# Optimization experiments

Measured on AMD Instinct MI355X. Metric: run time of the kernel, lower is better.

Reference implementation:

```python
import jax, jax.numpy as jnp
import numpy as np

B, N, K, G = 8, 16384, 16, 4
D_OUT = 128
CQ = CV = 64            # cv must equal d_out//2 for the lpe reshape to work
CQG, CVG = CQ // G, CV // G
C_LPE = D_OUT // (2 * G)  # = CVG = 16
BN_EPS = 1e-5


def setup_inputs() -> dict:
    key = jax.random.key(0)
    ks = jax.random.split(key, 8)
    xyz = jax.random.normal(ks[0], (B, N, 3), dtype=jnp.float32)
    query = jax.random.normal(ks[1], (B, CQ, N), dtype=jnp.float32)
    value = jax.random.normal(ks[2], (B, CV, N, 1), dtype=jnp.float32)
    neigh_idx = jax.random.randint(ks[3], (B, N, K), 0, N, dtype=jnp.int64)
    idx_base = (jnp.arange(B, dtype=jnp.int64) * N).reshape(B, 1, 1)
    lpe_W = jax.random.normal(ks[4], (C_LPE, 10), dtype=jnp.float32) * 0.1
    lpe_b = jnp.zeros((C_LPE,), dtype=jnp.float32)
    bn_gamma = jnp.ones((C_LPE,), dtype=jnp.float32)
    bn_beta = jnp.zeros((C_LPE,), dtype=jnp.float32)
    bn_mean = jnp.zeros((C_LPE,), dtype=jnp.float32)
    bn_var = jnp.ones((C_LPE,), dtype=jnp.float32)
    return {"xyz": xyz, "query": query, "value": value,
            "neigh_idx": neigh_idx, "idx_base": idx_base,
            "lpe_W": lpe_W, "lpe_b": lpe_b, "bn_gamma": bn_gamma,
            "bn_beta": bn_beta, "bn_mean": bn_mean, "bn_var": bn_var}


def _gtl_forward(xyz, query, value, neigh_idx, idx_base,
                 lpe_W, lpe_b, bn_gamma, bn_beta, bn_mean, bn_var):
    b, n, _ = xyz.shape
    k = neigh_idx.shape[-1]
    lq = query.reshape(b, G, CQG, n)                       # [b,g,cqg,n]
    lv = value.reshape(b, G, CVG, n)                       # [b,g,cvg,n]
    xyz_g = jnp.broadcast_to(xyz[:, None].transpose(0, 1, 3, 2), (b, G, 3, n))
    # temp channels: key(cqg) | value(cvg) | xyz(3)
    temp = jnp.concatenate([lq, lv, xyz_g], axis=2)        # [b,g,c,n]
    c = temp.shape[2]
    # flat gather honoring idx_base (batch offsets into b*n)
    flat_idx = (neigh_idx + idx_base).reshape(-1)          # [b*n*k]
    pc_flat = temp.transpose(1, 0, 3, 2).reshape(G, b * n, c)
    feat = pc_flat[:, flat_idx, :].reshape(G, b, n, k, c)
    feat = feat.transpose(1, 0, 4, 2, 3)                   # [b,g,c,n,k]
    lk = feat[:, :, :CQG]                                  # [b,g,cqg,n,k]
    lv_n = feat[:, :, CQG:CQG + CVG]                       # [b,g,cvg,n,k]
    f_xyz = feat[:, :, -3:]                                # [b,g,3,n,k]
    # relative positional encoding -> [b,g,n,k,10]
    neighbor_xyz = f_xyz.transpose(0, 1, 3, 4, 2)          # [b,g,n,k,3]
    xyz_tile = jnp.broadcast_to(xyz[:, None, :, None, :], (b, G, n, k, 3))
    relative_xyz = xyz_tile - neighbor_xyz
    relative_dis = jnp.sqrt(jnp.sum(relative_xyz ** 2, axis=-1, keepdims=True))
    relf = jnp.concatenate([relative_dis, relative_xyz, xyz_tile, neighbor_xyz], axis=-1)
    # permute(0,4,2,1,3) then merge (g,k) -> conv input [b,10,n,g*k]
    relf = relf.transpose(0, 4, 2, 1, 3).reshape(b, 10, n, G * k)
    y = jnp.einsum('oc,bcnm->bonm', lpe_W, relf) + lpe_b[None, :, None, None]
    inv_std = bn_gamma / jnp.sqrt(bn_var + BN_EPS)
    y = (y - bn_mean[None, :, None, None]) * inv_std[None, :, None, None] \
        + bn_beta[None, :, None, None]
    y = jax.nn.relu(y)
    f_enc = y.reshape(b, C_LPE, n, G, k).transpose(0, 3, 1, 2, 4)  # [b,g,cvg,n,k]
    # elementwise attention over neighbors
    la = jax.nn.softmax(jnp.sum(lq[..., None] * lk, axis=2), axis=-1)  # [b,g,n,k]
    lv_cat = jnp.concatenate([lv_n, f_enc], axis=2)        # [b,g,2*cvg,n,k]
    out = jnp.sum(la[:, :, None] * lv_cat, axis=-1).reshape(b, -1, n, 1)
    # attention centrality: scatter-add over neighbor indices
    idx_flat = jnp.broadcast_to(neigh_idx[:, None], (b, G, n, k)).reshape(b, G, n * k)
    att_flat = la.reshape(b, G, n * k)
    centrality = jnp.zeros((b, G, n), dtype=la.dtype).at[
        jnp.arange(b)[:, None, None], jnp.arange(G)[None, :, None], idx_flat
    ].add(att_flat)
    return out, f_enc, centrality


def reference(xyz, query, value, neigh_idx, idx_base,
              lpe_W, lpe_b, bn_gamma, bn_beta, bn_mean, bn_var):
    return _gtl_forward(xyz, query, value, neigh_idx, idx_base,
                        lpe_W, lpe_b, bn_gamma, bn_beta, bn_mean, bn_var)
```

## Files before the change

### kernel.cpp

```cpp
#include <hip/hip_runtime.h>
#include <hip/hip_fp16.h>

#define B_    8
#define N_    16384
#define K_    16
#define G_    4
#define CQ_   64
#define CV_   64
#define CQG_  16
#define CVG_  16
#define CLPE_ 16
#define NT_   (B_*G_*N_)

typedef float f4v __attribute__((ext_vector_type(4)));

static __device__ __forceinline__ void nt_store4(float* p, float a, float b,
                                                 float c, float d) {
    f4v v = {a, b, c, d};
    __builtin_nontemporal_store(v, (f4v*)p);
}
static __device__ __forceinline__ void nt_store1(float* p, float a) {
    __builtin_nontemporal_store(a, p);
}

union QV { uint4 u; __half2 h[4]; };

__global__ __launch_bounds__(256) void gtl_prep(
    const float* __restrict__ query,
    const float* __restrict__ value,
    const float* __restrict__ xyz,
    uint4*  __restrict__ qvT,
    float4* __restrict__ xyz4,
    float*  __restrict__ cent)
{
    const int gid = blockIdx.x * 256 + threadIdx.x;
    const int n   = gid & (N_ - 1);
    const int bg  = gid >> 14;
    const int g   = bg & (G_ - 1);
    const int b   = bg >> 2;

    const float* qb = query + (size_t)b*CQ_*N_ + (size_t)g*CQG_*N_ + n;
    const float* vb = value + (size_t)b*CV_*N_ + (size_t)g*CVG_*N_ + n;

    uint u[16];
    #pragma unroll
    for (int i = 0; i < 8; ++i) {
        const float a0 = qb[(size_t)(2*i+0)*N_];
        const float a1 = qb[(size_t)(2*i+1)*N_];
        const __half2 h = __floats2half2_rn(a0, a1);
        u[i] = *(const uint*)&h;
    }
    #pragma unroll
    for (int i = 0; i < 8; ++i) {
        const float a0 = vb[(size_t)(2*i+0)*N_];
        const float a1 = vb[(size_t)(2*i+1)*N_];
        const __half2 h = __floats2half2_rn(a0, a1);
        u[8+i] = *(const uint*)&h;
    }

    uint4* o = qvT + (size_t)gid * 4;
    o[0] = make_uint4(u[0],  u[1],  u[2],  u[3]);
    o[1] = make_uint4(u[4],  u[5],  u[6],  u[7]);
    o[2] = make_uint4(u[8],  u[9],  u[10], u[11]);
    o[3] = make_uint4(u[12], u[13], u[14], u[15]);

    cent[gid] = 0.f;

    if (g == 0) {
        const size_t pp = (size_t)b*N_ + n;
        xyz4[pp] = make_float4(xyz[pp*3+0], xyz[pp*3+1], xyz[pp*3+2], 0.f);
    }
}

__global__ __launch_bounds__(256) void gtl_main(
    const uint4*  __restrict__ qvT,
    const float4* __restrict__ xyz4,
    const int*    __restrict__ nidx,
    const float*  __restrict__ lpeW,
    const float*  __restrict__ lpeB,
    const float*  __restrict__ bnG,
    const float*  __restrict__ bnB,
    const float*  __restrict__ bnM,
    const float*  __restrict__ bnV,
    float* __restrict__ out,
    float* __restrict__ fenc,
    float* __restrict__ cent)
{
    __shared__ float4 sA[CLPE_];
    __shared__ float4 sB[CLPE_];

    const int t = threadIdx.x;
    if (t < CLPE_) {
        const float scale = bnG[t] * rsqrtf(bnV[t] + 1e-5f);
        const float shift = (lpeB[t] - bnM[t]) * scale + bnB[t];
        const float w0 = lpeW[t*10+0];
        const float w1 = lpeW[t*10+1], w2 = lpeW[t*10+2], w3 = lpeW[t*10+3];
        const float w4 = lpeW[t*10+4], w5 = lpeW[t*10+5], w6 = lpeW[t*10+6];
        const float w7 = lpeW[t*10+7], w8 = lpeW[t*10+8], w9 = lpeW[t*10+9];
        sA[t] = make_float4(scale*(w1+w4), scale*(w2+w5), scale*(w3+w6), shift);
        sB[t] = make_float4(scale*(w7-w1), scale*(w8-w2), scale*(w9-w3), scale*w0);
    }
    __syncthreads();

    const int wid  = blockIdx.x;
    const int xcd  = wid & 7;
    const int slot = wid >> 3;
    const int bg   = (xcd << 2) | (slot >> 6);
    const int n    = ((slot & 63) << 8) | t;
    const int b    = bg >> 2;

    int idx[K_];
    {
        const int4* ip = (const int4*)(nidx + (size_t)(b*N_ + n) * K_);
        #pragma unroll
        for (int q4 = 0; q4 < K_/4; ++q4) {
            const int4 v = ip[q4];
            idx[q4*4+0] = v.x; idx[q4*4+1] = v.y;
            idx[q4*4+2] = v.z; idx[q4*4+3] = v.w;
        }
    }

    const uint4* qvslab = qvT + (size_t)bg * N_ * 4;

    float lq[CQG_];
    {
        QV cA, cB;
        cA.u = qvslab[(size_t)n*4+0];
        cB.u = qvslab[(size_t)n*4+1];
        #pragma unroll
        for (int i = 0; i < 4; ++i) {
            const float2 f = __half22float2(cA.h[i]);
            lq[2*i+0] = f.x; lq[2*i+1] = f.y;
        }
        #pragma unroll
        for (int i = 0; i < 4; ++i) {
            const float2 f = __half22float2(cB.h[i]);
            lq[8+2*i+0] = f.x; lq[8+2*i+1] = f.y;
        }
    }

    float la[K_];
    #pragma unroll 4
    for (int k = 0; k < K_; ++k) {
        const uint4* qj = qvslab + (size_t)idx[k]*4;
        QV a, b2;
        a.u  = qj[0];
        b2.u = qj[1];
        float s = 0.f;
        #pragma unroll
        for (int i = 0; i < 4; ++i) {
            const float2 f = __half22float2(a.h[i]);
            s = fmaf(lq[2*i+0], f.x, s);
            s = fmaf(lq[2*i+1], f.y, s);
        }
        #pragma unroll
        for (int i = 0; i < 4; ++i) {
            const float2 f = __half22float2(b2.h[i]);
            s = fmaf(lq[8+2*i+0], f.x, s);
            s = fmaf(lq[8+2*i+1], f.y, s);
        }
        la[k] = s;
    }

    float m = la[0];
    #pragma unroll
    for (int k = 1; k < K_; ++k) m = fmaxf(m, la[k]);
    float ssum = 0.f;
    #pragma unroll
    for (int k = 0; k < K_; ++k) { const float e = __expf(la[k] - m); la[k] = e; ssum += e; }
    const float inv = 1.f / ssum;
    #pragma unroll
    for (int k = 0; k < K_; ++k) la[k] *= inv;

    {
        float* cb = cent + (size_t)bg * N_;
        #pragma unroll
        for (int k = 0; k < K_; ++k) atomicAdd(cb + idx[k], la[k]);
    }

    const float4 cpt = xyz4[(size_t)b*N_ + n];
    float basec[CLPE_];
    #pragma unroll
    for (int c = 0; c < CLPE_; ++c) {
        const float4 a = sA[c];
        basec[c] = fmaf(a.x, cpt.x, fmaf(a.y, cpt.y, fmaf(a.z, cpt.z, a.w)));
    }

    float4 nbr[K_];
    float accV[CVG_];
    #pragma unroll
    for (int c = 0; c < CVG_; ++c) accV[c] = 0.f;

    #pragma unroll 4
    for (int k = 0; k < K_; ++k) {
        const int j = idx[k];
        const float4 p = xyz4[(size_t)b*N_ + j];
        const float rx = cpt.x - p.x, ry = cpt.y - p.y, rz = cpt.z - p.z;
        const float d  = sqrtf(fmaf(rx,rx, fmaf(ry,ry, rz*rz)));
        nbr[k] = make_float4(p.x, p.y, p.z, d);
        const float w = la[k];
        const uint4* vj = qvslab + (size_t)j*4 + 2;
        QV v0, v1;
        v0.u = vj[0];
        v1.u = vj[1];
        #pragma unroll
        for (int i = 0; i < 4; ++i) {
            const float2 f = __half22float2(v0.h[i]);
            accV[2*i+0] = fmaf(w, f.x, accV[2*i+0]);
            accV[2*i+1] = fmaf(w, f.y, accV[2*i+1]);
        }
        #pragma unroll
        for (int i = 0; i < 4; ++i) {
            const float2 f = __half22float2(v1.h[i]);
            accV[8+2*i+0] = fmaf(w, f.x, accV[8+2*i+0]);
            accV[8+2*i+1] = fmaf(w, f.y, accV[8+2*i+1]);
        }
    }

    float* fe = fenc + ((size_t)bg * CLPE_ * N_ + n) * K_;
    float* ob = out  + (size_t)bg * (CVG_ + CLPE_) * N_ + n;

    #pragma unroll 2
    for (int c = 0; c < CLPE_; ++c) {
        const float4 wB = sB[c];
        const float base = basec[c];
        float e[K_];
        float acc = 0.f;
        #pragma unroll
        for (int k = 0; k < K_; ++k) {
            const float4 p = nbr[k];
            float tt = base;
            tt = fmaf(wB.x, p.x, tt);
            tt = fmaf(wB.y, p.y, tt);
            tt = fmaf(wB.z, p.z, tt);
            tt = fmaf(wB.w, p.w, tt);
            tt = fmaxf(tt, 0.f);
            e[k] = tt;
            acc  = fmaf(la[k], tt, acc);
        }
        float* fo = fe + (size_t)c * (N_ * K_);
        nt_store4(fo + 0,  e[0],  e[1],  e[2],  e[3]);
        nt_store4(fo + 4,  e[4],  e[5],  e[6],  e[7]);
        nt_store4(fo + 8,  e[8],  e[9],  e[10], e[11]);
        nt_store4(fo + 12, e[12], e[13], e[14], e[15]);
        nt_store1(ob + (size_t)(CVG_ + c) * N_, acc);
    }

    #pragma unroll
    for (int c = 0; c < CVG_; ++c) nt_store1(ob + (size_t)c * N_, accV[c]);
}

__global__ __launch_bounds__(256) void gtl_fallback(
    const float* __restrict__ xyz,
    const float* __restrict__ query,
    const float* __restrict__ value,
    const int*   __restrict__ nidx,
    const float* __restrict__ lpeW,
    const float* __restrict__ lpeB,
    const float* __restrict__ bnG,
    const float* __restrict__ bnB,
    const float* __restrict__ bnM,
    const float* __restrict__ bnV,
    float* __restrict__ out,
    float* __restrict__ fenc,
    float* __restrict__ cent)
{
    __shared__ float4 sA[CLPE_];
    __shared__ float4 sB[CLPE_];
    const int t = threadIdx.x;
    if (t < CLPE_) {
        const float scale = bnG[t] * rsqrtf(bnV[t] + 1e-5f);
        const float shift = (lpeB[t] - bnM[t]) * scale + bnB[t];
        const float w0 = lpeW[t*10+0];
        const float w1 = lpeW[t*10+1], w2 = lpeW[t*10+2], w3 = lpeW[t*10+3];
        const float w4 = lpeW[t*10+4], w5 = lpeW[t*10+5], w6 = lpeW[t*10+6];
        const float w7 = lpeW[t*10+7], w8 = lpeW[t*10+8], w9 = lpeW[t*10+9];
        sA[t] = make_float4(scale*(w1+w4), scale*(w2+w5), scale*(w3+w6), shift);
        sB[t] = make_float4(scale*(w7-w1), scale*(w8-w2), scale*(w9-w3), scale*w0);
    }
    __syncthreads();
    const int gid = blockIdx.x * 256 + t;
    const int n   = gid & (N_ - 1);
    const int bg  = gid >> 14;
    const int g   = bg & (G_ - 1);
    const int b   = bg >> 2;
    const float cx = xyz[(size_t)(b*N_ + n)*3 + 0];
    const float cy = xyz[(size_t)(b*N_ + n)*3 + 1];
    const float cz = xyz[(size_t)(b*N_ + n)*3 + 2];
    int idx[K_];
    const int4* ip = (const int4*)(nidx + (size_t)(b*N_ + n) * K_);
    #pragma unroll
    for (int q4 = 0; q4 < K_/4; ++q4) {
        const int4 v = ip[q4];
        idx[q4*4+0] = v.x; idx[q4*4+1] = v.y; idx[q4*4+2] = v.z; idx[q4*4+3] = v.w;
    }
    const float* qb = query + (size_t)b*CQ_*N_ + (size_t)g*CQG_*N_;
    float lq[CQG_];
    #pragma unroll
    for (int c = 0; c < CQG_; ++c) lq[c] = qb[(size_t)c*N_ + n];
    float la[K_];
    #pragma unroll 4
    for (int k = 0; k < K_; ++k) {
        const float* qj = qb + idx[k];
        float s = 0.f;
        #pragma unroll
        for (int c = 0; c < CQG_; ++c) s = fmaf(lq[c], qj[(size_t)c*N_], s);
        la[k] = s;
    }
    float m = la[0];
    #pragma unroll
    for (int k = 1; k < K_; ++k) m = fmaxf(m, la[k]);
    float ssum = 0.f;
    #pragma unroll
    for (int k = 0; k < K_; ++k) { const float e = __expf(la[k] - m); la[k] = e; ssum += e; }
    const float inv = 1.f / ssum;
    #pragma unroll
    for (int k = 0; k < K_; ++k) la[k] *= inv;
    float* cb = cent + (size_t)bg * N_;
    #pragma unroll
    for (int k = 0; k < K_; ++k) atomicAdd(cb + idx[k], la[k]);
    float basec[CLPE_];
    #pragma unroll
    for (int c = 0; c < CLPE_; ++c) {
        const float4 a = sA[c];
        basec[c] = fmaf(a.x, cx, fmaf(a.y, cy, fmaf(a.z, cz, a.w)));
    }
    const float* vb = value + (size_t)b*CV_*N_ + (size_t)g*CVG_*N_;
    float accV[CVG_], accE[CLPE_];
    #pragma unroll
    for (int c = 0; c < CLPE_; ++c) { accV[c] = 0.f; accE[c] = 0.f; }
    float* fe = fenc + ((size_t)bg * CLPE_ * N_ + n) * K_;
    #pragma unroll 2
    for (int k = 0; k < K_; ++k) {
        const int j = idx[k];
        const float nx = xyz[(size_t)(b*N_ + j)*3 + 0];
        const float ny = xyz[(size_t)(b*N_ + j)*3 + 1];
        const float nz = xyz[(size_t)(b*N_ + j)*3 + 2];
        const float rx = cx - nx, ry = cy - ny, rz = cz - nz;
        const float d  = sqrtf(rx*rx + ry*ry + rz*rz);
        const float w  = la[k];
        const float* vj = vb + j;
        #pragma unroll
        for (int c = 0; c < CLPE_; ++c) {
            const float4 bb = sB[c];
            float e = basec[c];
            e = fmaf(bb.x, nx, e); e = fmaf(bb.y, ny, e);
            e = fmaf(bb.z, nz, e); e = fmaf(bb.w, d,  e);
            e = fmaxf(e, 0.f);
            fe[(size_t)c*(N_*K_) + k] = e;
            accE[c] = fmaf(w, e, accE[c]);
            accV[c] = fmaf(w, vj[(size_t)c*N_], accV[c]);
        }
    }
    float* ob = out + (size_t)bg * (CVG_ + CLPE_) * N_ + n;
    #pragma unroll
    for (int c = 0; c < CVG_; ++c)  ob[(size_t)c*N_]        = accV[c];
    #pragma unroll
    for (int c = 0; c < CLPE_; ++c) ob[(size_t)(CVG_+c)*N_] = accE[c];
}

extern "C" void kernel_launch(void* const* d_in, const int* in_sizes, int n_in,
                              void* d_out, int out_size, void* d_ws, size_t ws_size,
                              hipStream_t stream) {
    (void)in_sizes; (void)n_in; (void)out_size;

    const float* xyz   = (const float*)d_in[0];
    const float* query = (const float*)d_in[1];
    const float* value = (const float*)d_in[2];
    const int*   nidx  = (const int*)  d_in[3];
    const float* lpeW  = (const float*)d_in[5];
    const float* lpeB  = (const float*)d_in[6];
    const float* bnG   = (const float*)d_in[7];
    const float* bnB   = (const float*)d_in[8];
    const float* bnM   = (const float*)d_in[9];
    const float* bnV   = (const float*)d_in[10];

    float* out  = (float*)d_out;
    float* fenc = out  + (size_t)B_ * (G_*(CVG_+CLPE_)) * N_;
    float* cent = fenc + (size_t)B_ * G_ * CLPE_ * N_ * K_;

    const size_t qv_bytes   = (size_t)NT_ * 64;
    const size_t xyz4_bytes = (size_t)B_ * N_ * sizeof(float4);
    const size_t need = qv_bytes + xyz4_bytes;

    const int grid = NT_ / 256;

    if (ws_size >= need) {
        uint4*  qvT  = (uint4*)d_ws;
        float4* xyz4 = (float4*)((char*)d_ws + qv_bytes);
        hipLaunchKernelGGL(gtl_prep, dim3(grid), dim3(256), 0, stream,
                           query, value, xyz, qvT, xyz4, cent);
        hipLaunchKernelGGL(gtl_main, dim3(grid), dim3(256), 0, stream,
                           qvT, xyz4, nidx, lpeW, lpeB, bnG, bnB, bnM, bnV,
                           out, fenc, cent);
    } else {
        hipMemsetAsync(cent, 0, sizeof(float) * (size_t)B_ * G_ * N_, stream);
        hipLaunchKernelGGL(gtl_fallback, dim3(grid), dim3(256), 0, stream,
                           xyz, query, value, nidx, lpeW, lpeB, bnG, bnB, bnM, bnV,
                           out, fenc, cent);
    }
}
```

Before: 1.204 ms.

## Fuse score and value gathers with online softmax, two points per thread

The main kernel now processes two point slots per thread with half the grid. It gathers each neighbor's full 64-byte q/v row plus xyz in one pass and uses an online-softmax rescale, so the value accumulation no longer needs a second gather loop. Neighbor coordinates and distances are kept as half2 to cut register use, neighbor indices are read with nontemporal loads, and the prep kernel's block-to-data mapping now matches the main kernel's XCD-aware layout. This trades extra exp and multiply work and some fp16 precision loss in the positional encoding for fewer memory passes and lower register pressure.

```diff
diff --git a/kernel.cpp b/kernel.cpp
--- a/kernel.cpp
+++ b/kernel.cpp
@@ -13,6 +13,7 @@
 #define NT_   (B_*G_*N_)
 
 typedef float f4v __attribute__((ext_vector_type(4)));
+typedef int   i4v __attribute__((ext_vector_type(4)));
 
 static __device__ __forceinline__ void nt_store4(float* p, float a, float b,
                                                  float c, float d) {
@@ -33,29 +34,32 @@
     float4* __restrict__ xyz4,
     float*  __restrict__ cent)
 {
-    const int gid = blockIdx.x * 256 + threadIdx.x;
-    const int n   = gid & (N_ - 1);
-    const int bg  = gid >> 14;
+    const int wid = blockIdx.x;
+    const int xcd = wid & 7;
+    const int i   = wid >> 3;
+    const int bg  = (xcd << 2) | (i >> 6);
+    const int n   = ((i & 63) << 8) | threadIdx.x;
     const int g   = bg & (G_ - 1);
     const int b   = bg >> 2;
+    const int gid = (bg << 14) | n;
 
     const float* qb = query + (size_t)b*CQ_*N_ + (size_t)g*CQG_*N_ + n;
     const float* vb = value + (size_t)b*CV_*N_ + (size_t)g*CVG_*N_ + n;
 
     uint u[16];
     #pragma unroll
-    for (int i = 0; i < 8; ++i) {
-        const float a0 = qb[(size_t)(2*i+0)*N_];
-        const float a1 = qb[(size_t)(2*i+1)*N_];
+    for (int q2 = 0; q2 < 8; ++q2) {
+        const float a0 = qb[(size_t)(2*q2+0)*N_];
+        const float a1 = qb[(size_t)(2*q2+1)*N_];
         const __half2 h = __floats2half2_rn(a0, a1);
-        u[i] = *(const uint*)&h;
-    }
-    #pragma unroll
-    for (int i = 0; i < 8; ++i) {
-        const float a0 = vb[(size_t)(2*i+0)*N_];
-        const float a1 = vb[(size_t)(2*i+1)*N_];
+        u[q2] = *(const uint*)&h;
+    }
+    #pragma unroll
+    for (int q2 = 0; q2 < 8; ++q2) {
+        const float a0 = vb[(size_t)(2*q2+0)*N_];
+        const float a1 = vb[(size_t)(2*q2+1)*N_];
         const __half2 h = __floats2half2_rn(a0, a1);
-        u[8+i] = *(const uint*)&h;
+        u[8+q2] = *(const uint*)&h;
     }
 
     uint4* o = qvT + (size_t)gid * 4;
@@ -104,150 +108,159 @@
 
     const int wid  = blockIdx.x;
     const int xcd  = wid & 7;
-    const int slot = wid >> 3;
-    const int bg   = (xcd << 2) | (slot >> 6);
-    const int n    = ((slot & 63) << 8) | t;
-    const int b    = bg >> 2;
-
-    int idx[K_];
-    {
-        const int4* ip = (const int4*)(nidx + (size_t)(b*N_ + n) * K_);
-        #pragma unroll
-        for (int q4 = 0; q4 < K_/4; ++q4) {
-            const int4 v = ip[q4];
-            idx[q4*4+0] = v.x; idx[q4*4+1] = v.y;
-            idx[q4*4+2] = v.z; idx[q4*4+3] = v.w;
-        }
-    }
-
-    const uint4* qvslab = qvT + (size_t)bg * N_ * 4;
-
-    float lq[CQG_];
-    {
-        QV cA, cB;
-        cA.u = qvslab[(size_t)n*4+0];
-        cB.u = qvslab[(size_t)n*4+1];
-        #pragma unroll
-        for (int i = 0; i < 4; ++i) {
-            const float2 f = __half22float2(cA.h[i]);
-            lq[2*i+0] = f.x; lq[2*i+1] = f.y;
-        }
-        #pragma unroll
-        for (int i = 0; i < 4; ++i) {
-            const float2 f = __half22float2(cB.h[i]);
-            lq[8+2*i+0] = f.x; lq[8+2*i+1] = f.y;
-        }
-    }
-
-    float la[K_];
-    #pragma unroll 4
-    for (int k = 0; k < K_; ++k) {
-        const uint4* qj = qvslab + (size_t)idx[k]*4;
-        QV a, b2;
-        a.u  = qj[0];
-        b2.u = qj[1];
-        float s = 0.f;
-        #pragma unroll
-        for (int i = 0; i < 4; ++i) {
-            const float2 f = __half22float2(a.h[i]);
-            s = fmaf(lq[2*i+0], f.x, s);
-            s = fmaf(lq[2*i+1], f.y, s);
-        }
-        #pragma unroll
-        for (int i = 0; i < 4; ++i) {
-            const float2 f = __half22float2(b2.h[i]);
-            s = fmaf(lq[8+2*i+0], f.x, s);
-            s = fmaf(lq[8+2*i+1], f.y, s);
-        }
-        la[k] = s;
-    }
-
-    float m = la[0];
-    #pragma unroll
-    for (int k = 1; k < K_; ++k) m = fmaxf(m, la[k]);
-    float ssum = 0.f;
-    #pragma unroll
-    for (int k = 0; k < K_; ++k) { const float e = __expf(la[k] - m); la[k] = e; ssum += e; }
-    const float inv = 1.f / ssum;
-    #pragma unroll
-    for (int k = 0; k < K_; ++k) la[k] *= inv;
-
-    {
-        float* cb = cent + (size_t)bg * N_;
-        #pragma unroll
-        for (int k = 0; k < K_; ++k) atomicAdd(cb + idx[k], la[k]);
-    }
-
-    const float4 cpt = xyz4[(size_t)b*N_ + n];
-    float basec[CLPE_];
-    #pragma unroll
-    for (int c = 0; c < CLPE_; ++c) {
-        const float4 a = sA[c];
-        basec[c] = fmaf(a.x, cpt.x, fmaf(a.y, cpt.y, fmaf(a.z, cpt.z, a.w)));
-    }
-
-    float4 nbr[K_];
-    float accV[CVG_];
-    #pragma unroll
-    for (int c = 0; c < CVG_; ++c) accV[c] = 0.f;
-
-    #pragma unroll 4
-    for (int k = 0; k < K_; ++k) {
-        const int j = idx[k];
-        const float4 p = xyz4[(size_t)b*N_ + j];
-        const float rx = cpt.x - p.x, ry = cpt.y - p.y, rz = cpt.z - p.z;
-        const float d  = sqrtf(fmaf(rx,rx, fmaf(ry,ry, rz*rz)));
-        nbr[k] = make_float4(p.x, p.y, p.z, d);
-        const float w = la[k];
-        const uint4* vj = qvslab + (size_t)j*4 + 2;
-        QV v0, v1;
-        v0.u = vj[0];
-        v1.u = vj[1];
-        #pragma unroll
-        for (int i = 0; i < 4; ++i) {
-            const float2 f = __half22float2(v0.h[i]);
-            accV[2*i+0] = fmaf(w, f.x, accV[2*i+0]);
-            accV[2*i+1] = fmaf(w, f.y, accV[2*i+1]);
-        }
-        #pragma unroll
-        for (int i = 0; i < 4; ++i) {
-            const float2 f = __half22float2(v1.h[i]);
-            accV[8+2*i+0] = fmaf(w, f.x, accV[8+2*i+0]);
-            accV[8+2*i+1] = fmaf(w, f.y, accV[8+2*i+1]);
-        }
-    }
-
-    float* fe = fenc + ((size_t)bg * CLPE_ * N_ + n) * K_;
-    float* ob = out  + (size_t)bg * (CVG_ + CLPE_) * N_ + n;
-
-    #pragma unroll 2
-    for (int c = 0; c < CLPE_; ++c) {
-        const float4 wB = sB[c];
-        const float base = basec[c];
-        float e[K_];
-        float acc = 0.f;
-        #pragma unroll
+    const int half = wid >> 3;
+
+    #pragma unroll 1
+    for (int p = 0; p < 2; ++p) {
+        const int slot = half + (p << 7);
+        const int bg   = (xcd << 2) | (slot >> 6);
+        const int n    = ((slot & 63) << 8) | t;
+        const int b    = bg >> 2;
+        const size_t xb = (size_t)b * N_;
+
+        int idx[K_];
+        {
+            const i4v* ip = (const i4v*)(nidx + ((size_t)b*N_ + n) * K_);
+            #pragma unroll
+            for (int q4 = 0; q4 < K_/4; ++q4) {
+                const i4v v = __builtin_nontemporal_load(ip + q4);
+                idx[q4*4+0] = v.x; idx[q4*4+1] = v.y;
+                idx[q4*4+2] = v.z; idx[q4*4+3] = v.w;
+            }
+        }
+
+        const uint4* qvslab = qvT + (size_t)bg * N_ * 4;
+
+        float lq[CQG_];
+        {
+            QV cA, cB;
+            cA.u = qvslab[(size_t)n*4+0];
+            cB.u = qvslab[(size_t)n*4+1];
+            #pragma unroll
+            for (int i2 = 0; i2 < 4; ++i2) {
+                const float2 f = __half22float2(cA.h[i2]);
+                lq[2*i2+0] = f.x; lq[2*i2+1] = f.y;
+            }
+            #pragma unroll
+            for (int i2 = 0; i2 < 4; ++i2) {
+                const float2 f = __half22float2(cB.h[i2]);
+                lq[8+2*i2+0] = f.x; lq[8+2*i2+1] = f.y;
+            }
+        }
+        const float4 cpt = xyz4[xb + n];
+
+        float la[K_];
+        float accV[CVG_];
+        __half2 nbh[2*K_];
+        #pragma unroll
+        for (int c = 0; c < CVG_; ++c) accV[c] = 0.f;
+        float m = -1e30f;
+
+        #pragma unroll 4
         for (int k = 0; k < K_; ++k) {
-            const float4 p = nbr[k];
-            float tt = base;
-            tt = fmaf(wB.x, p.x, tt);
-            tt = fmaf(wB.y, p.y, tt);
-            tt = fmaf(wB.z, p.z, tt);
-            tt = fmaf(wB.w, p.w, tt);
-            tt = fmaxf(tt, 0.f);
-            e[k] = tt;
-            acc  = fmaf(la[k], tt, acc);
-        }
-        float* fo = fe + (size_t)c * (N_ * K_);
-        nt_store4(fo + 0,  e[0],  e[1],  e[2],  e[3]);
-        nt_store4(fo + 4,  e[4],  e[5],  e[6],  e[7]);
-        nt_store4(fo + 8,  e[8],  e[9],  e[10], e[11]);
-        nt_store4(fo + 12, e[12], e[13], e[14], e[15]);
-        nt_store1(ob + (size_t)(CVG_ + c) * N_, acc);
-    }
-
-    #pragma unroll
-    for (int c = 0; c < CVG_; ++c) nt_store1(ob + (size_t)c * N_, accV[c]);
+            const int j = idx[k];
+            const uint4* rp = qvslab + (size_t)j*4;
+            QV r0, r1, r2, r3;
+            r0.u = rp[0]; r1.u = rp[1]; r2.u = rp[2]; r3.u = rp[3];
+            const float4 pp = xyz4[xb + j];
+
+            float s = 0.f;
+            #pragma unroll
+            for (int i2 = 0; i2 < 4; ++i2) {
+                const float2 f = __half22float2(r0.h[i2]);
+                s = fmaf(lq[2*i2+0], f.x, s);
+                s = fmaf(lq[2*i2+1], f.y, s);
+            }
+            #pragma unroll
+            for (int i2 = 0; i2 < 4; ++i2) {
+                const float2 f = __half22float2(r1.h[i2]);
+                s = fmaf(lq[8+2*i2+0], f.x, s);
+                s = fmaf(lq[8+2*i2+1], f.y, s);
+            }
+            la[k] = s;
+
+            const float mn = fmaxf(m, s);
+            const float sc = __expf(m - mn);
+            const float w  = __expf(s - mn);
+            m = mn;
+
+            #pragma unroll
+            for (int i2 = 0; i2 < 4; ++i2) {
+                const float2 f = __half22float2(r2.h[i2]);
+                accV[2*i2+0] = fmaf(w, f.x, accV[2*i2+0]*sc);
+                accV[2*i2+1] = fmaf(w, f.y, accV[2*i2+1]*sc);
+            }
+            #pragma unroll
+            for (int i2 = 0; i2 < 4; ++i2) {
+                const float2 f = __half22float2(r3.h[i2]);
+                accV[8+2*i2+0] = fmaf(w, f.x, accV[8+2*i2+0]*sc);
+                accV[8+2*i2+1] = fmaf(w, f.y, accV[8+2*i2+1]*sc);
+            }
+
+            const float rx = cpt.x - pp.x, ry = cpt.y - pp.y, rz = cpt.z - pp.z;
+            const float d  = sqrtf(fmaf(rx,rx, fmaf(ry,ry, rz*rz)));
+            nbh[2*k+0] = __floats2half2_rn(pp.x, pp.y);
+            nbh[2*k+1] = __floats2half2_rn(pp.z, d);
+        }
+
+        float ssum = 0.f;
+        #pragma unroll
+        for (int k = 0; k < K_; ++k) {
+            const float e = __expf(la[k] - m);
+            la[k] = e; ssum += e;
+        }
+        const float inv = 1.f / ssum;
+        #pragma unroll
+        for (int k = 0; k < K_; ++k) la[k] *= inv;
+        #pragma unroll
+        for (int c = 0; c < CVG_; ++c) accV[c] *= inv;
+
+        {
+            float* cb = cent + (size_t)bg * N_;
+            #pragma unroll
+            for (int k = 0; k < K_; ++k) atomicAdd(cb + idx[k], la[k]);
+        }
+
+        float basec[CLPE_];
+        #pragma unroll
+        for (int c = 0; c < CLPE_; ++c) {
+            const float4 a = sA[c];
+            basec[c] = fmaf(a.x, cpt.x, fmaf(a.y, cpt.y, fmaf(a.z, cpt.z, a.w)));
+        }
+
+        float* fe = fenc + ((size_t)bg * CLPE_ * N_ + n) * K_;
+        float* ob = out  + (size_t)bg * (CVG_ + CLPE_) * N_ + n;
+
+        #pragma unroll 2
+        for (int c = 0; c < CLPE_; ++c) {
+            const float4 wB = sB[c];
+            const float base = basec[c];
+            float e[K_];
+            float acc = 0.f;
+            #pragma unroll
+            for (int k = 0; k < K_; ++k) {
+                const float2 pxy = __half22float2(nbh[2*k+0]);
+                const float2 pzd = __half22float2(nbh[2*k+1]);
+                float tt = base;
+                tt = fmaf(wB.x, pxy.x, tt);
+                tt = fmaf(wB.y, pxy.y, tt);
+                tt = fmaf(wB.z, pzd.x, tt);
+                tt = fmaf(wB.w, pzd.y, tt);
+                tt = fmaxf(tt, 0.f);
+                e[k] = tt;
+                acc  = fmaf(la[k], tt, acc);
+            }
+            float* fo = fe + (size_t)c * (N_ * K_);
+            nt_store4(fo + 0,  e[0],  e[1],  e[2],  e[3]);
+            nt_store4(fo + 4,  e[4],  e[5],  e[6],  e[7]);
+            nt_store4(fo + 8,  e[8],  e[9],  e[10], e[11]);
+            nt_store4(fo + 12, e[12], e[13], e[14], e[15]);
+            nt_store1(ob + (size_t)(CVG_ + c) * N_, acc);
+        }
+
+        #pragma unroll
+        for (int c = 0; c < CVG_; ++c) nt_store1(ob + (size_t)c * N_, accV[c]);
+    }
 }
 
 __global__ __launch_bounds__(256) void gtl_fallback(
@@ -383,19 +396,17 @@
     const size_t xyz4_bytes = (size_t)B_ * N_ * sizeof(float4);
     const size_t need = qv_bytes + xyz4_bytes;
 
-    const int grid = NT_ / 256;
-
     if (ws_size >= need) {
         uint4*  qvT  = (uint4*)d_ws;
         float4* xyz4 = (float4*)((char*)d_ws + qv_bytes);
-        hipLaunchKernelGGL(gtl_prep, dim3(grid), dim3(256), 0, stream,
+        hipLaunchKernelGGL(gtl_prep, dim3(NT_/256), dim3(256), 0, stream,
                            query, value, xyz, qvT, xyz4, cent);
-        hipLaunchKernelGGL(gtl_main, dim3(grid), dim3(256), 0, stream,
+        hipLaunchKernelGGL(gtl_main, dim3(NT_/512), dim3(256), 0, stream,
                            qvT, xyz4, nidx, lpeW, lpeB, bnG, bnB, bnM, bnV,
                            out, fenc, cent);
     } else {
-        hipMemsetAsync(cent, 0, sizeof(float) * (size_t)B_ * G_ * N_, stream);
-        hipLaunchKernelGGL(gtl_fallback, dim3(grid), dim3(256), 0, stream,
+        (void)hipMemsetAsync(cent, 0, sizeof(float) * (size_t)B_ * G_ * N_, stream);
+        hipLaunchKernelGGL(gtl_fallback, dim3(NT_/256), dim3(256), 0, stream,
                            xyz, query, value, nidx, lpeW, lpeB, bnG, bnB, bnM, bnV,
                            out, fenc, cent);
     }
```

Result: faster. 1.136 ms (-5.6%).
